# Optimization experiments

Hardware: AMD Instinct MI355X
Metric: run time of the kernel (lower is better)

Reference implementation:

```python
import jax, jax.numpy as jnp
import numpy as np

B, N, C, H, M, CC = 8, 1024, 1280, 20, 77, 768
FF = 4 * C
AQ_BITS = 8
W_BITS = 8


def fq_sym(x, bits=AQ_BITS):
    # per-tensor symmetric fake quant with straight-through estimator
    qmax = 2.0 ** (bits - 1) - 1.0
    delta = jnp.maximum(jnp.max(jnp.abs(x)), 1e-8) / qmax
    q = jnp.clip(jnp.round(x / delta), -qmax - 1.0, qmax) * delta
    return x + jax.lax.stop_gradient(q - x)


def fq_zero(x, bits=W_BITS):
    # asymmetric, always_zero (zero point = 0): for softmax probs in [0,1]
    levels = 2.0 ** bits - 1.0
    delta = jnp.maximum(jnp.max(x), 1e-8) / levels
    q = jnp.clip(jnp.round(x / delta), 0.0, levels) * delta
    return x + jax.lax.stop_gradient(q - x)


def layer_norm(x, g, b, eps=1e-5):
    mu = jnp.mean(x, axis=-1, keepdims=True)
    var = jnp.var(x, axis=-1, keepdims=True)
    return (x - mu) * jax.lax.rsqrt(var + eps) * g + b


def attention(x, ctx, Wq, Wk, Wv, Wo, bo, heads):
    b, n, c = x.shape
    m = ctx.shape[1]
    dh = c // heads
    q = fq_sym(x @ Wq)
    k = fq_sym(ctx @ Wk)
    v = fq_sym(ctx @ Wv)
    q = q.reshape(b, n, heads, dh).transpose(0, 2, 1, 3)
    k = k.reshape(b, m, heads, dh).transpose(0, 2, 1, 3)
    v = v.reshape(b, m, heads, dh).transpose(0, 2, 1, 3)
    scores = jnp.einsum('bhnd,bhmd->bhnm', q, k) * (dh ** -0.5)
    w = jax.nn.softmax(scores, axis=-1)
    w = fq_zero(w)  # quantized softmax weights (forces explicit prob materialization)
    out = jnp.einsum('bhnm,bhmd->bhnd', w, v)
    out = out.transpose(0, 2, 1, 3).reshape(b, n, c)
    return out @ Wo + bo


def geglu_ff(x, W1, b1, W2, b2):
    h = x @ W1 + b1
    a, g = jnp.split(h, 2, axis=-1)
    return (a * jax.nn.gelu(g)) @ W2 + b2


def setup_inputs() -> dict:
    key = jax.random.key(0)
    ks = jax.random.split(key, 16)
    s = 0.02
    return {
        'x': jax.random.normal(ks[0], (B, N, C), jnp.float32),
        'ctx': jax.random.normal(ks[1], (B, M, CC), jnp.float32),
        'ln1_g': jnp.ones((C,), jnp.float32), 'ln1_b': jnp.zeros((C,), jnp.float32),
        'ln2_g': jnp.ones((C,), jnp.float32), 'ln2_b': jnp.zeros((C,), jnp.float32),
        'ln3_g': jnp.ones((C,), jnp.float32), 'ln3_b': jnp.zeros((C,), jnp.float32),
        'Wq1': jax.random.normal(ks[2], (C, C), jnp.float32) * s,
        'Wk1': jax.random.normal(ks[3], (C, C), jnp.float32) * s,
        'Wv1': jax.random.normal(ks[4], (C, C), jnp.float32) * s,
        'Wo1': jax.random.normal(ks[5], (C, C), jnp.float32) * s,
        'bo1': jnp.zeros((C,), jnp.float32),
        'Wq2': jax.random.normal(ks[6], (C, C), jnp.float32) * s,
        'Wk2': jax.random.normal(ks[7], (CC, C), jnp.float32) * s,
        'Wv2': jax.random.normal(ks[8], (CC, C), jnp.float32) * s,
        'Wo2': jax.random.normal(ks[9], (C, C), jnp.float32) * s,
        'bo2': jnp.zeros((C,), jnp.float32),
        'Wff1': jax.random.normal(ks[10], (C, 2 * FF), jnp.float32) * s,
        'bff1': jnp.zeros((2 * FF,), jnp.float32),
        'Wff2': jax.random.normal(ks[11], (FF, C), jnp.float32) * s,
        'bff2': jnp.zeros((C,), jnp.float32),
        'heads': H,
    }


def reference(x, ctx, ln1_g, ln1_b, ln2_g, ln2_b, ln3_g, ln3_b,
              Wq1, Wk1, Wv1, Wo1, bo1, Wq2, Wk2, Wv2, Wo2, bo2,
              Wff1, bff1, Wff2, bff2, heads):
    h = attention(layer_norm(x, ln1_g, ln1_b), layer_norm(x, ln1_g, ln1_b),
                  Wq1, Wk1, Wv1, Wo1, bo1, heads)
    x = x + h
    h = attention(layer_norm(x, ln2_g, ln2_b), ctx, Wq2, Wk2, Wv2, Wo2, bo2, heads)
    x = x + h
    x = x + geglu_ff(layer_norm(x, ln3_g, ln3_b), Wff1, bff1, Wff2, bff2)
    return x
```

## Files before the change

kernel.cpp:

```cpp
#include <hip/hip_runtime.h>

typedef __attribute__((ext_vector_type(8))) short bf16x8;
typedef __attribute__((ext_vector_type(4))) float f32x4;

#define DEV __device__ __forceinline__
#define MF(A, B, CACC) CACC = __builtin_amdgcn_mfma_f32_16x16x32_bf16(A, B, CACC, 0, 0, 0)

DEV ushort f2b(float f) {
  unsigned u = __float_as_uint(f);
  u += 0x7fffu + ((u >> 16) & 1u);
  return (ushort)(u >> 16);
}
DEV float b2f(ushort u) { return __uint_as_float(((unsigned)u) << 16); }

DEV void gl_lds16(ushort* lds_base, const ushort* gp) {
  __builtin_amdgcn_global_load_lds(
      (__attribute__((address_space(1))) const void*)gp,
      (__attribute__((address_space(3))) void*)lds_base, 16, 0, 0);
}

__global__ void k_zero(unsigned* p, int n) {
  int i = blockIdx.x * blockDim.x + threadIdx.x;
  if (i < n) p[i] = 0u;
}

__global__ __launch_bounds__(256) void k_wt(const float* __restrict__ W,
                                            ushort* __restrict__ WT, int K, int N) {
  __shared__ float T[32][33];
  int k0 = blockIdx.y * 32, n0 = blockIdx.x * 32;
  int tx = threadIdx.x & 31, ty = threadIdx.x >> 5;
  #pragma unroll
  for (int r = ty; r < 32; r += 8) {
    int k = k0 + r, n = n0 + tx;
    T[r][tx] = (k < K && n < N) ? W[(size_t)k * N + n] : 0.f;
  }
  __syncthreads();
  #pragma unroll
  for (int r = ty; r < 32; r += 8) {
    int n = n0 + r, k = k0 + tx;
    if (n < N && k < K) WT[(size_t)n * K + k] = f2b(T[tx][r]);
  }
}

__global__ void k_cvt(const float* __restrict__ in, ushort* __restrict__ out, int n) {
  int i = blockIdx.x * 256 + threadIdx.x;
  if (i < n) out[i] = f2b(in[i]);
}

__global__ __launch_bounds__(256) void k_ln(const float* __restrict__ x,
    const float* __restrict__ g, const float* __restrict__ b,
    ushort* __restrict__ out) {
  const int C = 1280;
  int row = blockIdx.x, tid = threadIdx.x;
  const float* xr = x + (size_t)row * C;
  float v0 = xr[tid], v1 = xr[tid + 256], v2 = xr[tid + 512],
        v3 = xr[tid + 768], v4 = xr[tid + 1024];
  float s = v0 + v1 + v2 + v3 + v4;
  float ss = v0 * v0 + v1 * v1 + v2 * v2 + v3 * v3 + v4 * v4;
  #pragma unroll
  for (int off = 32; off; off >>= 1) {
    s += __shfl_down(s, off);
    ss += __shfl_down(ss, off);
  }
  __shared__ float red[8];
  __shared__ float mu_s, rstd_s;
  int wave = tid >> 6, lane = tid & 63;
  if (lane == 0) { red[wave] = s; red[4 + wave] = ss; }
  __syncthreads();
  if (tid == 0) {
    float S = red[0] + red[1] + red[2] + red[3];
    float SS = red[4] + red[5] + red[6] + red[7];
    float mu = S / C;
    float var = SS / C - mu * mu;
    mu_s = mu;
    rstd_s = rsqrtf(var + 1e-5f);
  }
  __syncthreads();
  float mu = mu_s, rstd = rstd_s;
  size_t o = (size_t)row * C + tid;
  out[o]        = f2b((v0 - mu) * rstd * g[tid]        + b[tid]);
  out[o + 256]  = f2b((v1 - mu) * rstd * g[tid + 256]  + b[tid + 256]);
  out[o + 512]  = f2b((v2 - mu) * rstd * g[tid + 512]  + b[tid + 512]);
  out[o + 768]  = f2b((v3 - mu) * rstd * g[tid + 768]  + b[tid + 768]);
  out[o + 1024] = f2b((v4 - mu) * rstd * g[tid + 1024] + b[tid + 1024]);
}

DEV void st1(float v, int r_, int c_, int ldc, const float* resid,
             float* Cf, ushort* Cb) {
  size_t o = (size_t)r_ * ldc + c_;
  if (resid) v += resid[o];
  if (Cf) Cf[o] = v;
  if (Cb) Cb[o] = f2b(v);
}
DEV float epi4(f32x4 v, int rbase, int c_, int M, int N, int ldc,
               const float* bias, const float* resid, float* Cf, ushort* Cb) {
  float v0 = v.x, v1 = v.y, v2 = v.z, v3 = v.w;
  float am = fmaxf(fmaxf(fabsf(v0), fabsf(v1)), fmaxf(fabsf(v2), fabsf(v3)));
  if (c_ < N) {
    float bb = bias ? bias[c_] : 0.f;
    v0 += bb; v1 += bb; v2 += bb; v3 += bb;
    if (rbase + 0 < M) st1(v0, rbase + 0, c_, ldc, resid, Cf, Cb);
    if (rbase + 1 < M) st1(v1, rbase + 1, c_, ldc, resid, Cf, Cb);
    if (rbase + 2 < M) st1(v2, rbase + 2, c_, ldc, resid, Cf, Cb);
    if (rbase + 3 < M) st1(v3, rbase + 3, c_, ldc, resid, Cf, Cb);
  }
  return am;
}

__global__ __launch_bounds__(256) void k_gemm(
    const ushort* __restrict__ A, int lda,
    const ushort* __restrict__ BT, int ldb,
    float* __restrict__ Cf, ushort* __restrict__ Cb, int ldc,
    const float* __restrict__ bias, const float* __restrict__ resid,
    unsigned* am_slot, int M, int N, int K, int slcN) {
  __shared__ __align__(16) ushort SAB[8192];
  int tid = threadIdx.x;
  int wave = tid >> 6, lane = tid & 63;
  int q = lane >> 4, mi = lane & 15;
  int wr = (wave >> 1) * 64, wc = (wave & 1) * 64;
  int bm0 = blockIdx.y * 128, bn0 = blockIdx.x * 128;
  f32x4 c00 = {}, c01 = {}, c02 = {}, c03 = {};
  f32x4 c10 = {}, c11 = {}, c12 = {}, c13 = {};
  f32x4 c20 = {}, c21 = {}, c22 = {}, c23 = {};
  f32x4 c30 = {}, c31 = {}, c32 = {}, c33 = {};
  for (int k0 = 0; k0 < K; k0 += 32) {
    __syncthreads();
    #pragma unroll
    for (int t = 0; t < 4; t++) {
      int c = wave * 256 + t * 64 + lane;
      const ushort* gp;
      if (c < 512) {
        int r = c >> 2, kc = (c & 3) << 3;
        int gr = bm0 + r; if (gr >= M) gr = M - 1;
        gp = A + (size_t)gr * lda + k0 + kc;
      } else {
        int c2 = c - 512;
        int r = c2 >> 2, kc = (c2 & 3) << 3;
        int gn = bn0 + r; if (gn >= N) gn = N - 1;
        gp = BT + (size_t)gn * ldb + k0 + kc;
      }
      gl_lds16(&SAB[(wave * 256 + t * 64) * 8], gp);
    }
    __syncthreads();
    const ushort* Ab = &SAB[(wr + mi) * 32 + q * 8];
    const ushort* Bb = &SAB[4096 + (wc + mi) * 32 + q * 8];
    bf16x8 a0 = *(const bf16x8*)(Ab);
    bf16x8 a1 = *(const bf16x8*)(Ab + 512);
    bf16x8 a2 = *(const bf16x8*)(Ab + 1024);
    bf16x8 a3 = *(const bf16x8*)(Ab + 1536);
    bf16x8 b0 = *(const bf16x8*)(Bb);
    bf16x8 b1 = *(const bf16x8*)(Bb + 512);
    bf16x8 b2 = *(const bf16x8*)(Bb + 1024);
    bf16x8 b3 = *(const bf16x8*)(Bb + 1536);
    MF(a0, b0, c00); MF(a0, b1, c01); MF(a0, b2, c02); MF(a0, b3, c03);
    MF(a1, b0, c10); MF(a1, b1, c11); MF(a1, b2, c12); MF(a1, b3, c13);
    MF(a2, b0, c20); MF(a2, b1, c21); MF(a2, b2, c22); MF(a2, b3, c23);
    MF(a3, b0, c30); MF(a3, b1, c31); MF(a3, b2, c32); MF(a3, b3, c33);
  }
  int rb = bm0 + wr + q * 4, cb = bn0 + wc + mi;
  float am = 0.f;
  am = fmaxf(am, epi4(c00, rb +  0, cb +  0, M, N, ldc, bias, resid, Cf, Cb));
  am = fmaxf(am, epi4(c01, rb +  0, cb + 16, M, N, ldc, bias, resid, Cf, Cb));
  am = fmaxf(am, epi4(c02, rb +  0, cb + 32, M, N, ldc, bias, resid, Cf, Cb));
  am = fmaxf(am, epi4(c03, rb +  0, cb + 48, M, N, ldc, bias, resid, Cf, Cb));
  am = fmaxf(am, epi4(c10, rb + 16, cb +  0, M, N, ldc, bias, resid, Cf, Cb));
  am = fmaxf(am, epi4(c11, rb + 16, cb + 16, M, N, ldc, bias, resid, Cf, Cb));
  am = fmaxf(am, epi4(c12, rb + 16, cb + 32, M, N, ldc, bias, resid, Cf, Cb));
  am = fmaxf(am, epi4(c13, rb + 16, cb + 48, M, N, ldc, bias, resid, Cf, Cb));
  am = fmaxf(am, epi4(c20, rb + 32, cb +  0, M, N, ldc, bias, resid, Cf, Cb));
  am = fmaxf(am, epi4(c21, rb + 32, cb + 16, M, N, ldc, bias, resid, Cf, Cb));
  am = fmaxf(am, epi4(c22, rb + 32, cb + 32, M, N, ldc, bias, resid, Cf, Cb));
  am = fmaxf(am, epi4(c23, rb + 32, cb + 48, M, N, ldc, bias, resid, Cf, Cb));
  am = fmaxf(am, epi4(c30, rb + 48, cb +  0, M, N, ldc, bias, resid, Cf, Cb));
  am = fmaxf(am, epi4(c31, rb + 48, cb + 16, M, N, ldc, bias, resid, Cf, Cb));
  am = fmaxf(am, epi4(c32, rb + 48, cb + 32, M, N, ldc, bias, resid, Cf, Cb));
  am = fmaxf(am, epi4(c33, rb + 48, cb + 48, M, N, ldc, bias, resid, Cf, Cb));
  if (am_slot) {
    #pragma unroll
    for (int off = 32; off; off >>= 1) am = fmaxf(am, __shfl_down(am, off));
    if (lane == 0) atomicMax(am_slot + bn0 / slcN, __float_as_uint(am));
  }
}

__global__ void k_quant8(const ushort* __restrict__ in, ushort* __restrict__ out,
                         const unsigned* __restrict__ slotb, int n8,
                         int colw8, int ld, int slcw) {
  int i = blockIdx.x * 256 + threadIdx.x;
  if (i >= n8) return;
  int row = i / colw8, c8 = i - row * colw8;
  int col = c8 * 8;
  size_t a = (size_t)row * ld + col;
  float delta = fmaxf(__uint_as_float(slotb[col / slcw]), 1e-8f) * (1.f / 127.f);
  bf16x8 v = *(const bf16x8*)(in + a);
  bf16x8 r;
  #pragma unroll
  for (int j = 0; j < 8; j++) {
    float x = b2f((ushort)v[j]);
    float y = fminf(fmaxf(rintf(x / delta), -128.f), 127.f) * delta;
    r[j] = (short)f2b(y);
  }
  *(bf16x8*)(out + a) = r;
}

__global__ __launch_bounds__(256) void k_vt(const ushort* __restrict__ vq,
    ushort* __restrict__ vT, int H, int Mr, int Mpad, int ldv) {
  __shared__ __align__(16) ushort T[64][72];
  int bh = blockIdx.y, b = bh / H, h = bh % H;
  int m0 = blockIdx.x * 64;
  int tid = threadIdx.x;
  #pragma unroll
  for (int c = tid; c < 512; c += 256) {
    int mm = c >> 3, dc = (c & 7) << 3;
    int m = m0 + mm;
    int4 val = make_int4(0, 0, 0, 0);
    if (m < Mr) val = *(const int4*)(vq + ((size_t)b * Mr + m) * ldv + h * 64 + dc);
    *(int4*)&T[mm][dc] = val;
  }
  __syncthreads();
  #pragma unroll
  for (int c = tid; c < 512; c += 256) {
    int dd = c >> 3, mc = (c & 7) << 3;
    unsigned w0 = (unsigned)T[mc + 0][dd] | ((unsigned)T[mc + 1][dd] << 16);
    unsigned w1 = (unsigned)T[mc + 2][dd] | ((unsigned)T[mc + 3][dd] << 16);
    unsigned w2 = (unsigned)T[mc + 4][dd] | ((unsigned)T[mc + 5][dd] << 16);
    unsigned w3 = (unsigned)T[mc + 6][dd] | ((unsigned)T[mc + 7][dd] << 16);
    int4 val = make_int4((int)w0, (int)w1, (int)w2, (int)w3);
    *(int4*)(vT + ((size_t)bh * 64 + dd) * Mpad + m0 + mc) = val;
  }
}

#define NEGI -3.0e38f
#define VMA4 asm volatile("s_waitcnt vmcnt(4)" ::: "memory")
#define VMA2 asm volatile("s_waitcnt vmcnt(2)" ::: "memory")
#define VMA0 asm volatile("s_waitcnt vmcnt(0)" ::: "memory")
#define LGK0 asm volatile("s_waitcnt lgkmcnt(0)" ::: "memory")
#define RBAR __builtin_amdgcn_s_barrier()

#define ONLUPD(SA, SB, SC, SD, MRUN, ZRUN) do { \
  float e0  = b0_  ? (SA).x * cs : NEGI; \
  float e1  = b1_  ? (SA).y * cs : NEGI; \
  float e2  = b2_  ? (SA).z * cs : NEGI; \
  float e3  = b3_  ? (SA).w * cs : NEGI; \
  float e4  = b4_  ? (SB).x * cs : NEGI; \
  float e5  = b5_  ? (SB).y * cs : NEGI; \
  float e6  = b6_  ? (SB).z * cs : NEGI; \
  float e7  = b7_  ? (SB).w * cs : NEGI; \
  float e8  = b8_  ? (SC).x * cs : NEGI; \
  float e9  = b9_  ? (SC).y * cs : NEGI; \
  float e10 = b10_ ? (SC).z * cs : NEGI; \
  float e11 = b11_ ? (SC).w * cs : NEGI; \
  float e12 = b12_ ? (SD).x * cs : NEGI; \
  float e13 = b13_ ? (SD).y * cs : NEGI; \
  float e14 = b14_ ? (SD).z * cs : NEGI; \
  float e15 = b15_ ? (SD).w * cs : NEGI; \
  float tm = fmaxf(fmaxf(fmaxf(fmaxf(e0, e1), fmaxf(e2, e3)), \
                         fmaxf(fmaxf(e4, e5), fmaxf(e6, e7))), \
                   fmaxf(fmaxf(fmaxf(e8, e9), fmaxf(e10, e11)), \
                         fmaxf(fmaxf(e12, e13), fmaxf(e14, e15)))); \
  float mn = fmaxf(MRUN, tm); \
  float zs = exp2f(e0 - mn)  + exp2f(e1 - mn)  + exp2f(e2 - mn)  + exp2f(e3 - mn) \
           + exp2f(e4 - mn)  + exp2f(e5 - mn)  + exp2f(e6 - mn)  + exp2f(e7 - mn) \
           + exp2f(e8 - mn)  + exp2f(e9 - mn)  + exp2f(e10 - mn) + exp2f(e11 - mn) \
           + exp2f(e12 - mn) + exp2f(e13 - mn) + exp2f(e14 - mn) + exp2f(e15 - mn); \
  ZRUN = ZRUN * exp2f(MRUN - mn) + zs; MRUN = mn; \
} while (0)

__global__ __launch_bounds__(256) void k_attn1(
    const ushort* __restrict__ qq, const ushort* __restrict__ kq,
    float2* __restrict__ rs, unsigned* __restrict__ pmax,
    int H, int N, int Mr, int ldq, int ldk, float cs) {
  __shared__ __align__(16) ushort Qs[128][72];
  __shared__ __align__(16) ushort KL[2][4096];
  int tid = threadIdx.x;
  int wave = tid >> 6, lane = tid & 63;
  int q = lane >> 4, mi = lane & 15;
  int bh = blockIdx.y, b = bh / H, h = bh % H;
  int r0 = blockIdx.x * 128;
  #pragma unroll
  for (int c = tid; c < 1024; c += 256) {
    int r = c >> 3, dc = (c & 7) << 3;
    *(int4*)&Qs[r][dc] = *(const int4*)(qq + ((size_t)b * N + r0 + r) * ldq + h * 64 + dc);
  }
  int lr8 = lane >> 3;
  int ck = (lane & 7) ^ lr8;
  const ushort* kbase = kq + (size_t)b * Mr * ldk + h * 64 + ck * 8;
  auto stK = [&](int mt, int bb) {
    #pragma unroll
    for (int c = 0; c < 2; c++) {
      int base8 = c * 4 + wave;
      int m = mt * 64 + base8 * 8 + lr8; if (m >= Mr) m = Mr - 1;
      gl_lds16(&KL[bb][base8 * 512], kbase + (size_t)m * ldk);
    }
  };
  int nt = (Mr + 63) >> 6;
  stK(0, 0);
  if (nt > 1) { stK(1, 1); VMA2; } else VMA0;
  LGK0;
  RBAR;

  float m0r = NEGI, z0r = 0.f, m1r = NEGI, z1r = 0.f;
  int co0 = (q ^ (mi & 7)) * 8;
  int co1 = ((4 + q) ^ (mi & 7)) * 8;
  for (int mt = 0; mt < nt; mt++) {
    const ushort* KB = &KL[mt & 1][0];
    f32x4 s0 = {}, s1 = {}, s2 = {}, s3 = {};
    f32x4 s4 = {}, s5 = {}, s6 = {}, s7 = {};
    #pragma unroll
    for (int kc = 0; kc < 2; kc++) {
      int co = kc ? co1 : co0;
      bf16x8 qv0 = *(const bf16x8*)&Qs[wave * 32 + mi][kc * 32 + q * 8];
      bf16x8 qv1 = *(const bf16x8*)&Qs[wave * 32 + 16 + mi][kc * 32 + q * 8];
      bf16x8 k0v = *(const bf16x8*)&KB[mi * 64 + co];
      bf16x8 k1v = *(const bf16x8*)&KB[(16 + mi) * 64 + co];
      bf16x8 k2v = *(const bf16x8*)&KB[(32 + mi) * 64 + co];
      bf16x8 k3v = *(const bf16x8*)&KB[(48 + mi) * 64 + co];
      MF(k0v, qv0, s0); MF(k1v, qv0, s1); MF(k2v, qv0, s2); MF(k3v, qv0, s3);
      MF(k0v, qv1, s4); MF(k1v, qv1, s5); MF(k2v, qv1, s6); MF(k3v, qv1, s7);
    }
    int kb = mt * 64 + q * 4;
    bool b0_  = kb + 0  < Mr, b1_  = kb + 1  < Mr, b2_  = kb + 2  < Mr, b3_  = kb + 3  < Mr;
    bool b4_  = kb + 16 < Mr, b5_  = kb + 17 < Mr, b6_  = kb + 18 < Mr, b7_  = kb + 19 < Mr;
    bool b8_  = kb + 32 < Mr, b9_  = kb + 33 < Mr, b10_ = kb + 34 < Mr, b11_ = kb + 35 < Mr;
    bool b12_ = kb + 48 < Mr, b13_ = kb + 49 < Mr, b14_ = kb + 50 < Mr, b15_ = kb + 51 < Mr;
    ONLUPD(s0, s1, s2, s3, m0r, z0r);
    ONLUPD(s4, s5, s6, s7, m1r, z1r);
    RBAR;
    if (mt + 2 < nt) { stK(mt + 2, mt & 1); VMA2; }
    else VMA0;
    RBAR;
  }
  float mo0 = fmaxf(m0r, __shfl_xor(m0r, 16));
  mo0 = fmaxf(mo0, __shfl_xor(mo0, 32));
  float zz0 = z0r * exp2f(m0r - mo0);
  zz0 += __shfl_xor(zz0, 16);
  zz0 += __shfl_xor(zz0, 32);
  float mo1 = fmaxf(m1r, __shfl_xor(m1r, 16));
  mo1 = fmaxf(mo1, __shfl_xor(mo1, 32));
  float zz1 = z1r * exp2f(m1r - mo1);
  zz1 += __shfl_xor(zz1, 16);
  zz1 += __shfl_xor(zz1, 32);
  if (q == 0) {
    float2 st; st.x = mo0; st.y = zz0;
    rs[(size_t)bh * N + r0 + wave * 32 + mi] = st;
    st.x = mo1; st.y = zz1;
    rs[(size_t)bh * N + r0 + wave * 32 + 16 + mi] = st;
  }
  float pm = fmaxf(1.f / zz0, 1.f / zz1);
  #pragma unroll
  for (int off = 32; off; off >>= 1) pm = fmaxf(pm, __shfl_down(pm, off));
  if (lane == 0) atomicMax(pmax, __float_as_uint(pm));
}

DEV ushort q8lvl(float s, float cs, float mc) {
  float p = fminf(rintf(exp2f(fmaf(s, cs, -mc))), 255.f);
  return (ushort)(__float_as_uint(p) >> 16);
}

#define PWR(RB, SA, SB, SC, SD, M0_, M1_, M2_, M3_) do { \
  Ps[(RB) + 0][mi]      = ok0 ? q8lvl((SA).x, cs, M0_) : (ushort)0; \
  Ps[(RB) + 1][mi]      = ok0 ? q8lvl((SA).y, cs, M1_) : (ushort)0; \
  Ps[(RB) + 2][mi]      = ok0 ? q8lvl((SA).z, cs, M2_) : (ushort)0; \
  Ps[(RB) + 3][mi]      = ok0 ? q8lvl((SA).w, cs, M3_) : (ushort)0; \
  Ps[(RB) + 0][16 + mi] = ok1 ? q8lvl((SB).x, cs, M0_) : (ushort)0; \
  Ps[(RB) + 1][16 + mi] = ok1 ? q8lvl((SB).y, cs, M1_) : (ushort)0; \
  Ps[(RB) + 2][16 + mi] = ok1 ? q8lvl((SB).z, cs, M2_) : (ushort)0; \
  Ps[(RB) + 3][16 + mi] = ok1 ? q8lvl((SB).w, cs, M3_) : (ushort)0; \
  Ps[(RB) + 0][32 + mi] = ok2 ? q8lvl((SC).x, cs, M0_) : (ushort)0; \
  Ps[(RB) + 1][32 + mi] = ok2 ? q8lvl((SC).y, cs, M1_) : (ushort)0; \
  Ps[(RB) + 2][32 + mi] = ok2 ? q8lvl((SC).z, cs, M2_) : (ushort)0; \
  Ps[(RB) + 3][32 + mi] = ok2 ? q8lvl((SC).w, cs, M3_) : (ushort)0; \
  Ps[(RB) + 0][48 + mi] = ok3 ? q8lvl((SD).x, cs, M0_) : (ushort)0; \
  Ps[(RB) + 1][48 + mi] = ok3 ? q8lvl((SD).y, cs, M1_) : (ushort)0; \
  Ps[(RB) + 2][48 + mi] = ok3 ? q8lvl((SD).z, cs, M2_) : (ushort)0; \
  Ps[(RB) + 3][48 + mi] = ok3 ? q8lvl((SD).w, cs, M3_) : (ushort)0; \
} while (0)

#define OSTORE(RRBASE, OA, OB, OC, OD) do { \
  size_t base = ((size_t)b * N + (RRBASE)) * C + h * 64 + mi; \
  ao[base]              = f2b((OA).x * delta); ao[base + C]          = f2b((OA).y * delta); \
  ao[base + 2 * C]      = f2b((OA).z * delta); ao[base + 3 * C]      = f2b((OA).w * delta); \
  ao[base + 16]         = f2b((OB).x * delta); ao[base + C + 16]     = f2b((OB).y * delta); \
  ao[base + 2 * C + 16] = f2b((OB).z * delta); ao[base + 3 * C + 16] = f2b((OB).w * delta); \
  ao[base + 32]         = f2b((OC).x * delta); ao[base + C + 32]     = f2b((OC).y * delta); \
  ao[base + 2 * C + 32] = f2b((OC).z * delta); ao[base + 3 * C + 32] = f2b((OC).w * delta); \
  ao[base + 48]         = f2b((OD).x * delta); ao[base + C + 48]     = f2b((OD).y * delta); \
  ao[base + 2 * C + 48] = f2b((OD).z * delta); ao[base + 3 * C + 48] = f2b((OD).w * delta); \
} while (0)

__global__ __launch_bounds__(256) void k_attn2(
    const ushort* __restrict__ qq, const ushort* __restrict__ kq,
    const ushort* __restrict__ vT, const float2* __restrict__ rs,
    const unsigned* __restrict__ pmax, ushort* __restrict__ ao,
    int H, int N, int Mr, int Mpad, int ldq, int ldk, float cs) {
  const int C = 1280;
  __shared__ __align__(16) ushort Qs[128][72];
  __shared__ __align__(16) ushort Ps[128][72];
  __shared__ __align__(16) ushort KL[2][4096];
  __shared__ __align__(16) ushort VL[2][4096];
  int tid = threadIdx.x;
  int wave = tid >> 6, lane = tid & 63;
  int q = lane >> 4, mi = lane & 15;
  int bh = blockIdx.y, b = bh / H, h = bh % H;
  int r0 = blockIdx.x * 128;
  #pragma unroll
  for (int c = tid; c < 1024; c += 256) {
    int r = c >> 3, dc = (c & 7) << 3;
    *(int4*)&Qs[r][dc] = *(const int4*)(qq + ((size_t)b * N + r0 + r) * ldq + h * 64 + dc);
  }
  int lr8 = lane >> 3;
  int ck = (lane & 7) ^ lr8;
  const ushort* kbase = kq + (size_t)b * Mr * ldk + h * 64 + ck * 8;
  const ushort* vbase = vT + ((size_t)bh * 64) * Mpad + ck * 8;
  auto stKV = [&](int mt, int bb) {
    #pragma unroll
    for (int c = 0; c < 2; c++) {
      int base8 = c * 4 + wave;
      int rloc = base8 * 8 + lr8;
      int m = mt * 64 + rloc; if (m >= Mr) m = Mr - 1;
      gl_lds16(&KL[bb][base8 * 512], kbase + (size_t)m * ldk);
      gl_lds16(&VL[bb][base8 * 512], vbase + (size_t)rloc * Mpad + mt * 64);
    }
  };
  int rb0 = wave * 32 + q * 4, rb1 = rb0 + 16;
  float delta = fmaxf(__uint_as_float(*pmax), 1e-8f) * (1.f / 255.f);
  float ldl = __log2f(delta);
  float2 u0 = rs[(size_t)bh * N + r0 + rb0 + 0];
  float2 u1 = rs[(size_t)bh * N + r0 + rb0 + 1];
  float2 u2 = rs[(size_t)bh * N + r0 + rb0 + 2];
  float2 u3 = rs[(size_t)bh * N + r0 + rb0 + 3];
  float2 u4 = rs[(size_t)bh * N + r0 + rb1 + 0];
  float2 u5 = rs[(size_t)bh * N + r0 + rb1 + 1];
  float2 u6 = rs[(size_t)bh * N + r0 + rb1 + 2];
  float2 u7 = rs[(size_t)bh * N + r0 + rb1 + 3];
  float mc0 = u0.x + __log2f(u0.y) + ldl;
  float mc1 = u1.x + __log2f(u1.y) + ldl;
  float mc2 = u2.x + __log2f(u2.y) + ldl;
  float mc3 = u3.x + __log2f(u3.y) + ldl;
  float mc4 = u4.x + __log2f(u4.y) + ldl;
  float mc5 = u5.x + __log2f(u5.y) + ldl;
  float mc6 = u6.x + __log2f(u6.y) + ldl;
  float mc7 = u7.x + __log2f(u7.y) + ldl;
  int nt = (Mr + 63) >> 6;
  stKV(0, 0);
  if (nt > 1) { stKV(1, 1); VMA4; } else VMA0;
  LGK0;
  RBAR;

  f32x4 o0 = {}, o1 = {}, o2 = {}, o3 = {};
  f32x4 o4 = {}, o5 = {}, o6 = {}, o7 = {};
  int co0 = (q ^ (mi & 7)) * 8;
  int co1 = ((4 + q) ^ (mi & 7)) * 8;
  for (int mt = 0; mt < nt; mt++) {
    const ushort* KB = &KL[mt & 1][0];
    const ushort* VB = &VL[mt & 1][0];
    f32x4 s0 = {}, s1 = {}, s2 = {}, s3 = {};
    f32x4 s4 = {}, s5 = {}, s6 = {}, s7 = {};
    #pragma unroll
    for (int kc = 0; kc < 2; kc++) {
      int co = kc ? co1 : co0;
      bf16x8 aq0 = *(const bf16x8*)&Qs[wave * 32 + mi][kc * 32 + q * 8];
      bf16x8 aq1 = *(const bf16x8*)&Qs[wave * 32 + 16 + mi][kc * 32 + q * 8];
      bf16x8 k0v = *(const bf16x8*)&KB[mi * 64 + co];
      bf16x8 k1v = *(const bf16x8*)&KB[(16 + mi) * 64 + co];
      bf16x8 k2v = *(const bf16x8*)&KB[(32 + mi) * 64 + co];
      bf16x8 k3v = *(const bf16x8*)&KB[(48 + mi) * 64 + co];
      MF(aq0, k0v, s0); MF(aq0, k1v, s1); MF(aq0, k2v, s2); MF(aq0, k3v, s3);
      MF(aq1, k0v, s4); MF(aq1, k1v, s5); MF(aq1, k2v, s6); MF(aq1, k3v, s7);
    }
    int mlim = Mr - mt * 64;
    bool ok0 = (mi      < mlim);
    bool ok1 = (16 + mi < mlim);
    bool ok2 = (32 + mi < mlim);
    bool ok3 = (48 + mi < mlim);
    PWR(rb0, s0, s1, s2, s3, mc0, mc1, mc2, mc3);
    PWR(rb1, s4, s5, s6, s7, mc4, mc5, mc6, mc7);
    LGK0;
    __builtin_amdgcn_sched_barrier(0);
    #pragma unroll
    for (int kc = 0; kc < 2; kc++) {
      int co = kc ? co1 : co0;
      bf16x8 ap0 = *(const bf16x8*)&Ps[wave * 32 + mi][kc * 32 + q * 8];
      bf16x8 ap1 = *(const bf16x8*)&Ps[wave * 32 + 16 + mi][kc * 32 + q * 8];
      bf16x8 v0 = *(const bf16x8*)&VB[mi * 64 + co];
      bf16x8 v1 = *(const bf16x8*)&VB[(16 + mi) * 64 + co];
      bf16x8 v2 = *(const bf16x8*)&VB[(32 + mi) * 64 + co];
      bf16x8 v3 = *(const bf16x8*)&VB[(48 + mi) * 64 + co];
      MF(ap0, v0, o0); MF(ap0, v1, o1); MF(ap0, v2, o2); MF(ap0, v3, o3);
      MF(ap1, v0, o4); MF(ap1, v1, o5); MF(ap1, v2, o6); MF(ap1, v3, o7);
    }
    RBAR;
    if (mt + 2 < nt) { stKV(mt + 2, mt & 1); VMA4; }
    else VMA0;
    RBAR;
  }
  int rr0 = r0 + wave * 32 + q * 4;
  OSTORE(rr0, o0, o1, o2, o3);
  OSTORE(rr0 + 16, o4, o5, o6, o7);
}

#define BAR __builtin_amdgcn_s_barrier()
#define LGKM0 do { asm volatile("s_waitcnt lgkmcnt(0)" ::: "memory"); \
                   __builtin_amdgcn_sched_barrier(0); } while (0)
#define VM6 asm volatile("s_waitcnt vmcnt(6)" ::: "memory")
#define VM0 asm volatile("s_waitcnt vmcnt(0)" ::: "memory")
#define PRIO1 __builtin_amdgcn_s_setprio(1)
#define PRIO0 __builtin_amdgcn_s_setprio(0)

#define RDA01(P) do { \
  fa00 = *(const bf16x8*)&(P)[c0];        fa01 = *(const bf16x8*)&(P)[c1]; \
  fa10 = *(const bf16x8*)&(P)[1024 + c0]; fa11 = *(const bf16x8*)&(P)[1024 + c1]; } while (0)
#define RDA23(P) do { \
  fa20 = *(const bf16x8*)&(P)[2048 + c0]; fa21 = *(const bf16x8*)&(P)[2048 + c1]; \
  fa30 = *(const bf16x8*)&(P)[3072 + c0]; fa31 = *(const bf16x8*)&(P)[3072 + c1]; } while (0)
#define RDB(P, H) do { \
  b00 = *(const bf16x8*)&(P)[(H) + c0];        b01 = *(const bf16x8*)&(P)[(H) + c1]; \
  b10 = *(const bf16x8*)&(P)[(H) + 1024 + c0]; b11 = *(const bf16x8*)&(P)[(H) + 1024 + c1]; \
  b20 = *(const bf16x8*)&(P)[(H) + 2048 + c0]; b21 = *(const bf16x8*)&(P)[(H) + 2048 + c1]; \
  b30 = *(const bf16x8*)&(P)[(H) + 3072 + c0]; b31 = *(const bf16x8*)&(P)[(H) + 3072 + c1]; } while (0)
#define RDB8(P) RDB(P, 0)

#define MM8(AX0, AX1, AY0, AY1, C0, C1, C2, C3, D0, D1, D2, D3) \
  MF(AX0, b00, C0); MF(AX1, b01, C0); MF(AX0, b10, C1); MF(AX1, b11, C1); \
  MF(AX0, b20, C2); MF(AX1, b21, C2); MF(AX0, b30, C3); MF(AX1, b31, C3); \
  MF(AY0, b00, D0); MF(AY1, b01, D0); MF(AY0, b10, D1); MF(AY1, b11, D1); \
  MF(AY0, b20, D2); MF(AY1, b21, D2); MF(AY0, b30, D3); MF(AY1, b31, D3)

#define GB8(AP, BP, DB, KT) \
  RDA01(AP); RDB8(BP); \
  stB(DB, KT, 0); stB(DB, KT, 1); stA(DB, KT, 0); \
  BAR; LGKM0; \
  PRIO1; MM8(fa00, fa01, fa10, fa11, c00, c01, c02, c03, c10, c11, c12, c13); PRIO0; \
  BAR; \
  RDA23(AP); \
  stA(DB, KT, 1); stA(DB, KT, 2); stA(DB, KT, 3); \
  BAR; LGKM0; \
  PRIO1; MM8(fa20, fa21, fa30, fa31, c20, c21, c22, c23, c30, c31, c32, c33); PRIO0; \
  VM6; BAR;

#define GT8(AP, BP) \
  RDA01(AP); RDB8(BP); \
  BAR; LGKM0; \
  PRIO1; MM8(fa00, fa01, fa10, fa11, c00, c01, c02, c03, c10, c11, c12, c13); PRIO0; \
  BAR; \
  RDA23(AP); \
  BAR; LGKM0; \
  PRIO1; MM8(fa20, fa21, fa30, fa31, c20, c21, c22, c23, c30, c31, c32, c33); PRIO0;

__global__ __launch_bounds__(512) void k_gemm8(
    const ushort* __restrict__ A, int lda,
    const ushort* __restrict__ BT, int ldb,
    float* __restrict__ Cf, ushort* __restrict__ Cb, int ldc,
    const float* __restrict__ bias, const float* __restrict__ resid,
    unsigned* am_slot, int M, int N, int K, int slcN) {
  __shared__ __align__(16) ushort SAB[73728];
  int tid = threadIdx.x;
  int wave = tid >> 6, lane = tid & 63;
  int q = lane >> 4, mi = lane & 15;
  int wm = wave >> 1, wn = wave & 1;
  int lr = lane >> 3;
  int lc = ((lane & 7) ^ lr) * 8;

  int NBN = N >> 7;
  int nblk = (M >> 8) * NBN;
  int cpx = nblk >> 3;
  int wg = blockIdx.x;
  int swz = (wg & 7) * cpx + (wg >> 3);
  int bm0 = (swz / NBN) << 8, bn0 = (swz % NBN) << 7;

  const int swzr = (mi & 7) * 8;
  int c0 = (q * 8) ^ swzr, c1 = (32 + q * 8) ^ swzr;
  const ushort* A0p = &SAB[(wm * 64 + mi) * 64];
  const ushort* B0p = &SAB[16384 + (wn * 64 + mi) * 64];
  const ushort* A1p = A0p + 24576; const ushort* B1p = B0p + 24576;
  const ushort* A2p = A0p + 49152; const ushort* B2p = B0p + 49152;

  const ushort* gA = A  + (size_t)(bm0 + wave * 8 + lr) * lda + lc;
  const ushort* gB = BT + (size_t)(bn0 + wave * 8 + lr) * ldb + lc;
  ushort* lA = &SAB[wave * 512];
  ushort* lB = &SAB[16384 + wave * 512];

  auto stA = [&](int bb, int kt, int call) {
    gl_lds16(lA + bb * 24576 + call * 4096,
             gA + (size_t)call * 64 * lda + (size_t)kt * 64);
  };
  auto stB = [&](int bb, int kt, int call) {
    gl_lds16(lB + bb * 24576 + call * 4096,
             gB + (size_t)call * 64 * ldb + (size_t)kt * 64);
  };

  f32x4 c00 = {}, c01 = {}, c02 = {}, c03 = {};
  f32x4 c10 = {}, c11 = {}, c12 = {}, c13 = {};
  f32x4 c20 = {}, c21 = {}, c22 = {}, c23 = {};
  f32x4 c30 = {}, c31 = {}, c32 = {}, c33 = {};
  bf16x8 fa00, fa01, fa10, fa11, fa20, fa21, fa30, fa31;
  bf16x8 b00, b01, b10, b11, b20, b21, b30, b31;

  stB(0, 0, 0); stB(0, 0, 1);
  stA(0, 0, 0); stA(0, 0, 1); stA(0, 0, 2); stA(0, 0, 3);
  stB(1, 1, 0); stB(1, 1, 1);
  stA(1, 1, 0); stA(1, 1, 1); stA(1, 1, 2); stA(1, 1, 3);
  VM6; BAR;

  int NT = K >> 6, NTm = NT - 2;
  for (int t = 0; t < NTm; t += 3) {
    GB8(A0p, B0p, 2, t + 2);
    GB8(A1p, B1p, 0, t + 3);
    GB8(A2p, B2p, 1, t + 4);
  }
  GT8(A0p, B0p);
  VM0; BAR;
  GT8(A1p, B1p);

  int rb = bm0 + wm * 64 + q * 4, cb = bn0 + wn * 64 + mi;
  float am = 0.f;
  am = fmaxf(am, epi4(c00, rb +  0, cb +  0, M, N, ldc, bias, resid, Cf, Cb));
  am = fmaxf(am, epi4(c01, rb +  0, cb + 16, M, N, ldc, bias, resid, Cf, Cb));
  am = fmaxf(am, epi4(c02, rb +  0, cb + 32, M, N, ldc, bias, resid, Cf, Cb));
  am = fmaxf(am, epi4(c03, rb +  0, cb + 48, M, N, ldc, bias, resid, Cf, Cb));
  am = fmaxf(am, epi4(c10, rb + 16, cb +  0, M, N, ldc, bias, resid, Cf, Cb));
  am = fmaxf(am, epi4(c11, rb + 16, cb + 16, M, N, ldc, bias, resid, Cf, Cb));
  am = fmaxf(am, epi4(c12, rb + 16, cb + 32, M, N, ldc, bias, resid, Cf, Cb));
  am = fmaxf(am, epi4(c13, rb + 16, cb + 48, M, N, ldc, bias, resid, Cf, Cb));
  am = fmaxf(am, epi4(c20, rb + 32, cb +  0, M, N, ldc, bias, resid, Cf, Cb));
  am = fmaxf(am, epi4(c21, rb + 32, cb + 16, M, N, ldc, bias, resid, Cf, Cb));
  am = fmaxf(am, epi4(c22, rb + 32, cb + 32, M, N, ldc, bias, resid, Cf, Cb));
  am = fmaxf(am, epi4(c23, rb + 32, cb + 48, M, N, ldc, bias, resid, Cf, Cb));
  am = fmaxf(am, epi4(c30, rb + 48, cb +  0, M, N, ldc, bias, resid, Cf, Cb));
  am = fmaxf(am, epi4(c31, rb + 48, cb + 16, M, N, ldc, bias, resid, Cf, Cb));
  am = fmaxf(am, epi4(c32, rb + 48, cb + 32, M, N, ldc, bias, resid, Cf, Cb));
  am = fmaxf(am, epi4(c33, rb + 48, cb + 48, M, N, ldc, bias, resid, Cf, Cb));
  if (am_slot) {
    #pragma unroll
    for (int off = 32; off; off >>= 1) am = fmaxf(am, __shfl_down(am, off));
    if (lane == 0) atomicMax(am_slot + bn0 / slcN, __float_as_uint(am));
  }
}

DEV ushort ggel(float a, float g) {
  float u = 1.5957691216057308f * g * (1.f + 0.044715f * g * g);
  float s = 1.f / (1.f + __expf(-u));
  return f2b(a * g * s);
}
DEV void epi4g(f32x4 va, f32x4 vg, size_t base, float ba, float bg,
               ushort* __restrict__ GG) {
  GG[base]         = ggel(va.x + ba, vg.x + bg);
  GG[base + 5120]  = ggel(va.y + ba, vg.y + bg);
  GG[base + 10240] = ggel(va.z + ba, vg.z + bg);
  GG[base + 15360] = ggel(va.w + ba, vg.w + bg);
}
#define EPIN(nn, P0, Q0, P1, Q1, P2, Q2, P3, Q3) do { \
  int cg = colBase + nn * 16 + mi; \
  float ba = bias[cg], bg = bias[5120 + cg]; \
  size_t b0_ = (size_t)rowBase * 5120 + cg; \
  epi4g(P0, Q0, b0_,             ba, bg, GG); \
  epi4g(P1, Q1, b0_ + 16 * 5120, ba, bg, GG); \
  epi4g(P2, Q2, b0_ + 32 * 5120, ba, bg, GG); \
  epi4g(P3, Q3, b0_ + 48 * 5120, ba, bg, GG); \
} while (0)

__global__ __launch_bounds__(512) void k_ff1_8p(
    const ushort* __restrict__ A,
    const ushort* __restrict__ BT,
    const float* __restrict__ bias,
    ushort* __restrict__ GG) {
  __shared__ __align__(16) ushort SAB[65536];
  int tid = threadIdx.x;
  int wave = tid >> 6, lane = tid & 63;
  int q = lane >> 4, mi = lane & 15;
  int wm = wave >> 1, wn = wave & 1;
  int lr = lane >> 3;
  int lc = ((lane & 7) ^ lr) * 8;

  int wg = blockIdx.x;
  int swz = (wg & 7) * 160 + (wg >> 3);
  int bm0 = (swz & 31) * 256, bn0 = (swz >> 5) * 128;

  const int swzr = (mi & 7) * 8;
  int c0 = (q * 8) ^ swzr, c1 = (32 + q * 8) ^ swzr;
  const ushort* A0p = &SAB[(wm * 64 + mi) * 64];
  const ushort* B0p = &SAB[16384 + (wn * 64 + mi) * 64];
  const ushort* A1p = A0p + 32768;
  const ushort* B1p = B0p + 32768;

  const ushort* gA  = A  + (size_t)(bm0 + wave * 8 + lr) * 1280 + lc;
  const ushort* gBa = BT + (size_t)(bn0 + wave * 8 + lr) * 1280 + lc;
  const ushort* gBg = BT + (size_t)(5120 + bn0 + wave * 8 + lr) * 1280 + lc;
  ushort* lA = &SAB[wave * 512];
  ushort* lB = &SAB[16384 + wave * 512];

  auto stA = [&](int bb, int kt, int call) {
    gl_lds16(lA + bb * 32768 + call * 4096,
             gA + (size_t)call * 81920 + (size_t)kt * 64);
  };
  auto stBa = [&](int bb, int kt, int call) {
    gl_lds16(lB + bb * 32768 + call * 4096,
             gBa + (size_t)call * 81920 + (size_t)kt * 64);
  };
  auto stBg = [&](int bb, int kt, int call) {
    gl_lds16(lB + bb * 32768 + (call + 2) * 4096,
             gBg + (size_t)call * 81920 + (size_t)kt * 64);
  };

  f32x4 cA00 = {}, cA01 = {}, cA02 = {}, cA03 = {};
  f32x4 cA10 = {}, cA11 = {}, cA12 = {}, cA13 = {};
  f32x4 cA20 = {}, cA21 = {}, cA22 = {}, cA23 = {};
  f32x4 cA30 = {}, cA31 = {}, cA32 = {}, cA33 = {};
  f32x4 cG00 = {}, cG01 = {}, cG02 = {}, cG03 = {};
  f32x4 cG10 = {}, cG11 = {}, cG12 = {}, cG13 = {};
  f32x4 cG20 = {}, cG21 = {}, cG22 = {}, cG23 = {};
  f32x4 cG30 = {}, cG31 = {}, cG32 = {}, cG33 = {};
  bf16x8 fa00, fa01, fa10, fa11, fa20, fa21, fa30, fa31;
  bf16x8 b00, b01, b10, b11, b20, b21, b30, b31;

  stBa(0, 0, 0); stBa(0, 0, 1); stBg(0, 0, 0); stBg(0, 0, 1);
  stA(0, 0, 0); stA(0, 0, 1); stA(0, 0, 2); stA(0, 0, 3);
  stBa(1, 1, 0); stBa(1, 1, 1);
  stA(1, 1, 0); stA(1, 1, 1); stA(1, 1, 2); stA(1, 1, 3);
  VM6; BAR;

  for (int it = 0; it < 10; ++it) {
    int t1 = 2 * it + 1;
    int s0 = t1 + 1; if (s0 > 19) s0 = 19;
    int s1 = t1 + 2; if (s1 > 19) s1 = 19;
    RDA01(A0p); RDB(B0p, 0);
    stBg(1, t1, 0); stBg(1, t1, 1);
    BAR; LGKM0;
    PRIO1; MM8(fa00, fa01, fa10, fa11, cA00, cA01, cA02, cA03,
               cA10, cA11, cA12, cA13); PRIO0;
    BAR;
    RDA23(A0p);
    stBa(0, s0, 0); stBa(0, s0, 1);
    BAR; LGKM0;
    PRIO1; MM8(fa20, fa21, fa30, fa31, cA20, cA21, cA22, cA23,
               cA30, cA31, cA32, cA33); PRIO0;
    BAR;
    RDB(B0p, 8192);
    stA(0, s0, 0); stA(0, s0, 1);
    BAR; LGKM0;
    PRIO1; MM8(fa00, fa01, fa10, fa11, cG00, cG01, cG02, cG03,
               cG10, cG11, cG12, cG13); PRIO0;
    BAR;
    stA(0, s0, 2); stA(0, s0, 3);
    BAR;
    PRIO1; MM8(fa20, fa21, fa30, fa31, cG20, cG21, cG22, cG23,
               cG30, cG31, cG32, cG33); PRIO0;
    VM6; BAR;
    RDA01(A1p); RDB(B1p, 0);
    stBg(0, s0, 0); stBg(0, s0, 1);
    BAR; LGKM0;
    PRIO1; MM8(fa00, fa01, fa10, fa11, cA00, cA01, cA02, cA03,
               cA10, cA11, cA12, cA13); PRIO0;
    BAR;
    RDA23(A1p);
    stBa(1, s1, 0); stBa(1, s1, 1);
    BAR; LGKM0;
    PRIO1; MM8(fa20, fa21, fa30, fa31, cA20, cA21, cA22, cA23,
               cA30, cA31, cA32, cA33); PRIO0;
    BAR;
    RDB(B1p, 8192);
    stA(1, s1, 0); stA(1, s1, 1);
    BAR; LGKM0;
    PRIO1; MM8(fa00, fa01, fa10, fa11, cG00, cG01, cG02, cG03,
               cG10, cG11, cG12, cG13); PRIO0;
    BAR;
    stA(1, s1, 2); stA(1, s1, 3);
    BAR;
    PRIO1; MM8(fa20, fa21, fa30, fa31, cG20, cG21, cG22, cG23,
               cG30, cG31, cG32, cG33); PRIO0;
    VM6; BAR;
  }

  int colBase = bn0 + wn * 64;
  int rowBase = bm0 + wm * 64 + q * 4;
  EPIN(0, cA00, cG00, cA10, cG10, cA20, cG20, cA30, cG30);
  EPIN(1, cA01, cG01, cA11, cG11, cA21, cG21, cA31, cG31);
  EPIN(2, cA02, cG02, cA12, cG12, cA22, cG22, cA32, cG32);
  EPIN(3, cA03, cG03, cA13, cG13, cA23, cG23, cA33, cG33);
}

extern "C" void kernel_launch(void* const* d_in, const int* in_sizes, int n_in,
                              void* d_out, int out_size, void* d_ws, size_t ws_size,
                              hipStream_t stream) {
  const float* x_in = (const float*)d_in[0];
  const float* ctx  = (const float*)d_in[1];
  const float* ln1g = (const float*)d_in[2];
  const float* ln1b = (const float*)d_in[3];
  const float* ln2g = (const float*)d_in[4];
  const float* ln2b = (const float*)d_in[5];
  const float* ln3g = (const float*)d_in[6];
  const float* ln3b = (const float*)d_in[7];
  const float* Wq1  = (const float*)d_in[8];
  const float* Wk1  = (const float*)d_in[9];
  const float* Wv1  = (const float*)d_in[10];
  const float* Wo1  = (const float*)d_in[11];
  const float* bo1  = (const float*)d_in[12];
  const float* Wq2  = (const float*)d_in[13];
  const float* Wk2  = (const float*)d_in[14];
  const float* Wv2  = (const float*)d_in[15];
  const float* Wo2  = (const float*)d_in[16];
  const float* bo2  = (const float*)d_in[17];
  const float* Wff1 = (const float*)d_in[18];
  const float* bff1 = (const float*)d_in[19];
  const float* Wff2 = (const float*)d_in[20];
  const float* bff2 = (const float*)d_in[21];
  float* out = (float*)d_out;

  const int NR = 8192;
  const int C = 1280, H = 20, Nseq = 1024, CC = 768;
  const int MR2 = 616;
  const float CS = 0.18033688011112042f;

  char* ws = (char*)d_ws;
  size_t off = 0;
  auto alloc = [&](size_t bytes) -> void* {
    void* p = ws + off;
    off += (bytes + 255) & ~(size_t)255;
    return p;
  };
  unsigned* scal = (unsigned*)alloc(64);
  ushort* Wq1T  = (ushort*)alloc((size_t)C * C * 2);
  ushort* Wk1T  = (ushort*)alloc((size_t)C * C * 2);
  ushort* Wv1T  = (ushort*)alloc((size_t)C * C * 2);
  ushort* Wo1T  = (ushort*)alloc((size_t)C * C * 2);
  ushort* Wq2T  = (ushort*)alloc((size_t)C * C * 2);
  ushort* Wk2T  = (ushort*)alloc((size_t)C * CC * 2);
  ushort* Wv2T  = (ushort*)alloc((size_t)C * CC * 2);
  ushort* Wo2T  = (ushort*)alloc((size_t)C * C * 2);
  ushort* WF1T  = (ushort*)alloc((size_t)10240 * C * 2);
  ushort* WF2T  = (ushort*)alloc((size_t)C * 5120 * 2);
  ushort* LN    = (ushort*)alloc((size_t)NR * C * 2);
  size_t regionR = off;
  ushort* QKV   = (ushort*)alloc((size_t)NR * 3840 * 2);
  ushort* VT    = (ushort*)alloc((size_t)160 * 64 * 1024 * 2);
  float2* RS    = (float2*)alloc((size_t)160 * 1024 * 8);
  ushort* CTXB  = (ushort*)alloc((size_t)MR2 * CC * 2);
  ushort* KV2   = (ushort*)alloc((size_t)MR2 * 2560 * 2);
  size_t need = off;
  ushort* AO = LN;
  ushort* GG = (ushort*)(ws + regionR);
  if (ws_size < need) return;

  k_zero<<<1, 64, 0, stream>>>(scal, 8);
  k_wt<<<dim3(40, 40), 256, 0, stream>>>(Wq1, Wq1T, C, C);
  k_wt<<<dim3(40, 40), 256, 0, stream>>>(Wk1, Wk1T, C, C);
  k_wt<<<dim3(40, 40), 256, 0, stream>>>(Wv1, Wv1T, C, C);
  k_wt<<<dim3(40, 40), 256, 0, stream>>>(Wo1, Wo1T, C, C);
  k_wt<<<dim3(40, 40), 256, 0, stream>>>(Wq2, Wq2T, C, C);
  k_wt<<<dim3(40, 24), 256, 0, stream>>>(Wk2, Wk2T, CC, C);
  k_wt<<<dim3(40, 24), 256, 0, stream>>>(Wv2, Wv2T, CC, C);
  k_wt<<<dim3(40, 40), 256, 0, stream>>>(Wo2, Wo2T, C, C);
  k_wt<<<dim3(320, 40), 256, 0, stream>>>(Wff1, WF1T, C, 10240);
  k_wt<<<dim3(40, 160), 256, 0, stream>>>(Wff2, WF2T, 5120, C);

  k_ln<<<NR, 256, 0, stream>>>(x_in, ln1g, ln1b, LN);
  k_gemm8<<<dim3(960), 512, 0, stream>>>(LN, C, Wq1T, C, nullptr, QKV, 3840,
                                         nullptr, nullptr, scal + 0, NR, 3840, C, 1280);
  k_quant8<<<(NR * 3840 / 8 + 255) / 256, 256, 0, stream>>>(QKV, QKV, scal + 0,
                                                            NR * 480, 480, 3840, 1280);
  k_vt<<<dim3(16, 160), 256, 0, stream>>>(QKV + 2560, VT, H, 1024, 1024, 3840);
  k_attn1<<<dim3(8, 160), 256, 0, stream>>>(QKV, QKV + 1280, RS, scal + 3,
                                            H, Nseq, 1024, 3840, 3840, CS);
  k_attn2<<<dim3(8, 160), 256, 0, stream>>>(QKV, QKV + 1280, VT, RS, scal + 3, AO,
                                            H, Nseq, 1024, 1024, 3840, 3840, CS);
  k_gemm8<<<dim3(320), 512, 0, stream>>>(AO, C, Wo1T, C, out, nullptr, C,
                                         bo1, x_in, nullptr, NR, C, C, C);

  k_ln<<<NR, 256, 0, stream>>>(out, ln2g, ln2b, LN);
  k_gemm8<<<dim3(320), 512, 0, stream>>>(LN, C, Wq2T, C, nullptr, QKV, 3840,
                                         nullptr, nullptr, scal + 4, NR, C, C, C);
  k_quant8<<<(NR * C / 8 + 255) / 256, 256, 0, stream>>>(QKV, QKV, scal + 4,
                                                         NR * 160, 160, 3840, 1280);
  k_cvt<<<(MR2 * CC + 255) / 256, 256, 0, stream>>>(ctx, CTXB, MR2 * CC);
  k_gemm<<<dim3(20, 5), 256, 0, stream>>>(CTXB, CC, Wk2T, CC, nullptr, KV2, 2560,
                                          nullptr, nullptr, scal + 5, MR2, 2560, CC, 1280);
  k_quant8<<<(MR2 * 2560 / 8 + 255) / 256, 256, 0, stream>>>(KV2, KV2, scal + 5,
                                                             MR2 * 320, 320, 2560, 1280);
  k_vt<<<dim3(2, 160), 256, 0, stream>>>(KV2 + 1280, VT, H, 77, 128, 2560);
  k_attn1<<<dim3(8, 160), 256, 0, stream>>>(QKV, KV2, RS, scal + 7,
                                            H, Nseq, 77, 3840, 2560, CS);
  k_attn2<<<dim3(8, 160), 256, 0, stream>>>(QKV, KV2, VT, RS, scal + 7, AO,
                                            H, Nseq, 77, 128, 3840, 2560, CS);
  k_gemm8<<<dim3(320), 512, 0, stream>>>(AO, C, Wo2T, C, out, nullptr, C,
                                         bo2, out, nullptr, NR, C, C, C);

  k_ln<<<NR, 256, 0, stream>>>(out, ln3g, ln3b, LN);
  k_ff1_8p<<<dim3(1280), 512, 0, stream>>>(LN, WF1T, bff1, GG);
  k_gemm8<<<dim3(320), 512, 0, stream>>>(GG, 5120, WF2T, 5120, out, nullptr, C,
                                         bff2, out, nullptr, NR, C, 5120, C);
}
```

Measured before the change: 1.544 ms.

## Fuse Q/V fake-quant into attention loads and batch weight transposes into one launch

Removes the standalone quantization passes over Q and V. Q is now quantized when attention loads it into shared memory, and V is quantized inside the transpose kernel. Only K still goes through a separate, narrower quant kernel. The ten weight-transpose launches and the scalar-zeroing kernel are merged into one job-table kernel. This cuts full-tensor read/write passes and launch overhead, but attn1 and attn2 now each requantize Q redundantly.

Result: faster. 1.483 ms (median of 2 runs) (-3.9%).

```diff
diff --git a/kernel.cpp b/kernel.cpp
--- a/kernel.cpp
+++ b/kernel.cpp
@@ -19,15 +19,35 @@
       (__attribute__((address_space(3))) void*)lds_base, 16, 0, 0);
 }
 
-__global__ void k_zero(unsigned* p, int n) {
-  int i = blockIdx.x * blockDim.x + threadIdx.x;
-  if (i < n) p[i] = 0u;
-}
-
-__global__ __launch_bounds__(256) void k_wt(const float* __restrict__ W,
-                                            ushort* __restrict__ WT, int K, int N) {
+DEV int4 q8v(int4 val, float dq) {
+  ushort* p = (ushort*)&val;
+  #pragma unroll
+  for (int j = 0; j < 8; j++) {
+    float x = b2f(p[j]);
+    float y = fminf(fmaxf(rintf(x / dq), -128.f), 127.f) * dq;
+    p[j] = f2b(y);
+  }
+  return val;
+}
+
+struct WtJobs {
+  const float* W[10];
+  ushort* WT[10];
+  int Kd[10], Nd[10], nbx[10], bend[10];
+};
+__global__ __launch_bounds__(256) void k_wtb(WtJobs jb, unsigned* scal) {
+  if (blockIdx.x == 0 && threadIdx.x < 8) scal[threadIdx.x] = 0u;
+  int bid = blockIdx.x;
+  int i = 0;
+  while (bid >= jb.bend[i]) i++;
+  int base = i ? jb.bend[i - 1] : 0;
+  int local = bid - base;
+  int nbx = jb.nbx[i];
+  int k0 = (local / nbx) * 32, n0 = (local % nbx) * 32;
+  const float* __restrict__ W = jb.W[i];
+  ushort* __restrict__ WT = jb.WT[i];
+  int K = jb.Kd[i], N = jb.Nd[i];
   __shared__ float T[32][33];
-  int k0 = blockIdx.y * 32, n0 = blockIdx.x * 32;
   int tx = threadIdx.x & 31, ty = threadIdx.x >> 5;
   #pragma unroll
   for (int r = ty; r < 32; r += 8) {
@@ -203,17 +223,20 @@
 }
 
 __global__ __launch_bounds__(256) void k_vt(const ushort* __restrict__ vq,
-    ushort* __restrict__ vT, int H, int Mr, int Mpad, int ldv) {
+    ushort* __restrict__ vT, const unsigned* __restrict__ slot,
+    int H, int Mr, int Mpad, int ldv) {
   __shared__ __align__(16) ushort T[64][72];
   int bh = blockIdx.y, b = bh / H, h = bh % H;
   int m0 = blockIdx.x * 64;
   int tid = threadIdx.x;
+  float dq = fmaxf(__uint_as_float(*slot), 1e-8f) * (1.f / 127.f);
   #pragma unroll
   for (int c = tid; c < 512; c += 256) {
     int mm = c >> 3, dc = (c & 7) << 3;
     int m = m0 + mm;
     int4 val = make_int4(0, 0, 0, 0);
-    if (m < Mr) val = *(const int4*)(vq + ((size_t)b * Mr + m) * ldv + h * 64 + dc);
+    if (m < Mr)
+      val = q8v(*(const int4*)(vq + ((size_t)b * Mr + m) * ldv + h * 64 + dc), dq);
     *(int4*)&T[mm][dc] = val;
   }
   __syncthreads();
@@ -268,6 +291,7 @@
 __global__ __launch_bounds__(256) void k_attn1(
     const ushort* __restrict__ qq, const ushort* __restrict__ kq,
     float2* __restrict__ rs, unsigned* __restrict__ pmax,
+    const unsigned* __restrict__ qslot,
     int H, int N, int Mr, int ldq, int ldk, float cs) {
   __shared__ __align__(16) ushort Qs[128][72];
   __shared__ __align__(16) ushort KL[2][4096];
@@ -276,10 +300,12 @@
   int q = lane >> 4, mi = lane & 15;
   int bh = blockIdx.y, b = bh / H, h = bh % H;
   int r0 = blockIdx.x * 128;
+  float dqq = fmaxf(__uint_as_float(*qslot), 1e-8f) * (1.f / 127.f);
   #pragma unroll
   for (int c = tid; c < 1024; c += 256) {
     int r = c >> 3, dc = (c & 7) << 3;
-    *(int4*)&Qs[r][dc] = *(const int4*)(qq + ((size_t)b * N + r0 + r) * ldq + h * 64 + dc);
+    int4 val = *(const int4*)(qq + ((size_t)b * N + r0 + r) * ldq + h * 64 + dc);
+    *(int4*)&Qs[r][dc] = q8v(val, dqq);
   }
   int lr8 = lane >> 3;
   int ck = (lane & 7) ^ lr8;
@@ -390,7 +416,8 @@
 __global__ __launch_bounds__(256) void k_attn2(
     const ushort* __restrict__ qq, const ushort* __restrict__ kq,
     const ushort* __restrict__ vT, const float2* __restrict__ rs,
-    const unsigned* __restrict__ pmax, ushort* __restrict__ ao,
+    const unsigned* __restrict__ pmax, const unsigned* __restrict__ qslot,
+    ushort* __restrict__ ao,
     int H, int N, int Mr, int Mpad, int ldq, int ldk, float cs) {
   const int C = 1280;
   __shared__ __align__(16) ushort Qs[128][72];
@@ -402,10 +429,12 @@
   int q = lane >> 4, mi = lane & 15;
   int bh = blockIdx.y, b = bh / H, h = bh % H;
   int r0 = blockIdx.x * 128;
+  float dqq = fmaxf(__uint_as_float(*qslot), 1e-8f) * (1.f / 127.f);
   #pragma unroll
   for (int c = tid; c < 1024; c += 256) {
     int r = c >> 3, dc = (c & 7) << 3;
-    *(int4*)&Qs[r][dc] = *(const int4*)(qq + ((size_t)b * N + r0 + r) * ldq + h * 64 + dc);
+    int4 val = *(const int4*)(qq + ((size_t)b * N + r0 + r) * ldq + h * 64 + dc);
+    *(int4*)&Qs[r][dc] = q8v(val, dqq);
   }
   int lr8 = lane >> 3;
   int ck = (lane & 7) ^ lr8;
@@ -840,46 +869,51 @@
   ushort* GG = (ushort*)(ws + regionR);
   if (ws_size < need) return;
 
-  k_zero<<<1, 64, 0, stream>>>(scal, 8);
-  k_wt<<<dim3(40, 40), 256, 0, stream>>>(Wq1, Wq1T, C, C);
-  k_wt<<<dim3(40, 40), 256, 0, stream>>>(Wk1, Wk1T, C, C);
-  k_wt<<<dim3(40, 40), 256, 0, stream>>>(Wv1, Wv1T, C, C);
-  k_wt<<<dim3(40, 40), 256, 0, stream>>>(Wo1, Wo1T, C, C);
-  k_wt<<<dim3(40, 40), 256, 0, stream>>>(Wq2, Wq2T, C, C);
-  k_wt<<<dim3(40, 24), 256, 0, stream>>>(Wk2, Wk2T, CC, C);
-  k_wt<<<dim3(40, 24), 256, 0, stream>>>(Wv2, Wv2T, CC, C);
-  k_wt<<<dim3(40, 40), 256, 0, stream>>>(Wo2, Wo2T, C, C);
-  k_wt<<<dim3(320, 40), 256, 0, stream>>>(Wff1, WF1T, C, 10240);
-  k_wt<<<dim3(40, 160), 256, 0, stream>>>(Wff2, WF2T, 5120, C);
+  WtJobs jb;
+  auto setj = [&](int i, const float* W, ushort* WT, int K, int N) {
+    jb.W[i] = W; jb.WT[i] = WT; jb.Kd[i] = K; jb.Nd[i] = N;
+    jb.nbx[i] = (N + 31) / 32;
+    int nb = jb.nbx[i] * ((K + 31) / 32);
+    jb.bend[i] = (i ? jb.bend[i - 1] : 0) + nb;
+  };
+  setj(0, Wq1, Wq1T, C, C);
+  setj(1, Wk1, Wk1T, C, C);
+  setj(2, Wv1, Wv1T, C, C);
+  setj(3, Wo1, Wo1T, C, C);
+  setj(4, Wq2, Wq2T, C, C);
+  setj(5, Wk2, Wk2T, CC, C);
+  setj(6, Wv2, Wv2T, CC, C);
+  setj(7, Wo2, Wo2T, C, C);
+  setj(8, Wff1, WF1T, C, 10240);
+  setj(9, Wff2, WF2T, 5120, C);
+  k_wtb<<<dim3(jb.bend[9]), 256, 0, stream>>>(jb, scal);
 
   k_ln<<<NR, 256, 0, stream>>>(x_in, ln1g, ln1b, LN);
   k_gemm8<<<dim3(960), 512, 0, stream>>>(LN, C, Wq1T, C, nullptr, QKV, 3840,
                                          nullptr, nullptr, scal + 0, NR, 3840, C, 1280);
-  k_quant8<<<(NR * 3840 / 8 + 255) / 256, 256, 0, stream>>>(QKV, QKV, scal + 0,
-                                                            NR * 480, 480, 3840, 1280);
-  k_vt<<<dim3(16, 160), 256, 0, stream>>>(QKV + 2560, VT, H, 1024, 1024, 3840);
-  k_attn1<<<dim3(8, 160), 256, 0, stream>>>(QKV, QKV + 1280, RS, scal + 3,
+  k_quant8<<<(NR * 160 + 255) / 256, 256, 0, stream>>>(QKV + 1280, QKV + 1280, scal + 1,
+                                                       NR * 160, 160, 3840, 1280);
+  k_vt<<<dim3(16, 160), 256, 0, stream>>>(QKV + 2560, VT, scal + 2, H, 1024, 1024, 3840);
+  k_attn1<<<dim3(8, 160), 256, 0, stream>>>(QKV, QKV + 1280, RS, scal + 3, scal + 0,
                                             H, Nseq, 1024, 3840, 3840, CS);
-  k_attn2<<<dim3(8, 160), 256, 0, stream>>>(QKV, QKV + 1280, VT, RS, scal + 3, AO,
-                                            H, Nseq, 1024, 1024, 3840, 3840, CS);
+  k_attn2<<<dim3(8, 160), 256, 0, stream>>>(QKV, QKV + 1280, VT, RS, scal + 3, scal + 0,
+                                            AO, H, Nseq, 1024, 1024, 3840, 3840, CS);
   k_gemm8<<<dim3(320), 512, 0, stream>>>(AO, C, Wo1T, C, out, nullptr, C,
                                          bo1, x_in, nullptr, NR, C, C, C);
 
   k_ln<<<NR, 256, 0, stream>>>(out, ln2g, ln2b, LN);
   k_gemm8<<<dim3(320), 512, 0, stream>>>(LN, C, Wq2T, C, nullptr, QKV, 3840,
                                          nullptr, nullptr, scal + 4, NR, C, C, C);
-  k_quant8<<<(NR * C / 8 + 255) / 256, 256, 0, stream>>>(QKV, QKV, scal + 4,
-                                                         NR * 160, 160, 3840, 1280);
   k_cvt<<<(MR2 * CC + 255) / 256, 256, 0, stream>>>(ctx, CTXB, MR2 * CC);
   k_gemm<<<dim3(20, 5), 256, 0, stream>>>(CTXB, CC, Wk2T, CC, nullptr, KV2, 2560,
                                           nullptr, nullptr, scal + 5, MR2, 2560, CC, 1280);
-  k_quant8<<<(MR2 * 2560 / 8 + 255) / 256, 256, 0, stream>>>(KV2, KV2, scal + 5,
-                                                             MR2 * 320, 320, 2560, 1280);
-  k_vt<<<dim3(2, 160), 256, 0, stream>>>(KV2 + 1280, VT, H, 77, 128, 2560);
-  k_attn1<<<dim3(8, 160), 256, 0, stream>>>(QKV, KV2, RS, scal + 7,
+  k_quant8<<<(MR2 * 160 + 255) / 256, 256, 0, stream>>>(KV2, KV2, scal + 5,
+                                                        MR2 * 160, 160, 2560, 1280);
+  k_vt<<<dim3(2, 160), 256, 0, stream>>>(KV2 + 1280, VT, scal + 6, H, 77, 128, 2560);
+  k_attn1<<<dim3(8, 160), 256, 0, stream>>>(QKV, KV2, RS, scal + 7, scal + 4,
                                             H, Nseq, 77, 3840, 2560, CS);
-  k_attn2<<<dim3(8, 160), 256, 0, stream>>>(QKV, KV2, VT, RS, scal + 7, AO,
-                                            H, Nseq, 77, 128, 3840, 2560, CS);
+  k_attn2<<<dim3(8, 160), 256, 0, stream>>>(QKV, KV2, VT, RS, scal + 7, scal + 4,
+                                            AO, H, Nseq, 77, 128, 3840, 2560, CS);
   k_gemm8<<<dim3(320), 512, 0, stream>>>(AO, C, Wo2T, C, out, nullptr, C,
                                          bo2, out, nullptr, NR, C, C, C);
 
```
